# Kernel optimization log

Measured on AMD Instinct MI355X. Metric: run time of the kernel, lower is better.

The kernel has to match this reference:

```python
import jax, jax.numpy as jnp
import numpy as np

B, T, I, H = 64, 188, 512, 1024
R = H  # recurrent_size == hidden_size (required for the cell math to be consistent)


def setup_inputs() -> dict:
    key = jax.random.key(0)
    ks = jax.random.split(key, 6)
    stdv = 1.0 / np.sqrt(H)
    u = lambda k, shape: jax.random.uniform(k, shape, jnp.float32, -stdv, stdv)
    return {
        "x": jax.random.normal(ks[0], (B, T, I), jnp.float32),
        "h0": jnp.zeros((B, R), jnp.float32),
        "c0": jnp.zeros((B, H), jnp.float32),
        "weight_ih": u(ks[1], (4 * H, I)),
        "weight_hh": u(ks[2], (4 * H, R)),
        "weight_rec": u(ks[3], (2 * R, H)),
        "bias": u(ks[4], (4 * H,)),
        "lengths": jax.random.randint(ks[5], (B,), 1, T + 1),
    }


def reference(x, h0, c0, weight_ih, weight_hh, weight_rec, bias, lengths):
    # length_matrix[j][t] == 1 iff t < lengths[j]; state is zeroed where 0
    mask = (jnp.arange(T)[:, None] < lengths[None, :]).astype(x.dtype)[:, :, None]  # [T,B,1]
    # precompute input projections for all timesteps: [T, B, 4H]
    pre_x = jnp.einsum('bti,gi->tbg', x, weight_ih) + bias

    def step(carry, inp):
        h, c = carry
        px, m = inp
        pre = px + h @ weight_hh.T           # [B, 4H]
        pre_c = c @ weight_rec.T             # [B, 2R] (peephole)
        i = jax.nn.sigmoid(pre[:, :H] + pre_c[:, :H])
        f = jax.nn.sigmoid(pre[:, H:2 * H] + pre_c[:, H:2 * H])
        g = jnp.tanh(pre[:, 2 * H:3 * H])
        c_new = f * c + i * g
        o = jax.nn.sigmoid(pre[:, 3 * H:] + c_new)
        h_new = o * jnp.tanh(c_new)
        h_new = h_new * m  # zero finished sequences (index_fill_ with 0)
        c_new = c_new * m
        return (h_new, c_new), (h_new, c_new)

    (_, _), (hs, cs) = jax.lax.scan(step, (h0, c0), (pre_x, mask))
    # stack over time then transpose(0,1) as in torch -> [B, T, H]
    return jnp.swapaxes(hs, 0, 1), jnp.swapaxes(cs, 0, 1)
```

## Files before the change

kernel.cpp:

```cpp
#include <hip/hip_runtime.h>


#define T_N 188

#define WS_PX     0UL
#define WS_XB     98566144UL
#define WS_WIHB   110886912UL
#define WS_WCOMB  115081216UL
#define WS_HST    127664128UL
#define WS_CST    127926272UL
#define WS_FLAGS  128188416UL
#define WS_WRECLO 128192512UL
#define WS_CSTLO  132386816UL

typedef __attribute__((ext_vector_type(8))) short short8;
typedef __attribute__((ext_vector_type(4))) float f4;

__device__ __forceinline__ float b2f(unsigned short u) {
    union { unsigned int i; float f; } v; v.i = ((unsigned int)u) << 16; return v.f;
}
__device__ __forceinline__ unsigned short f2b(float f) {
    unsigned int u = __float_as_uint(f);
    return (unsigned short)((u + 0x7FFFu + ((u >> 16) & 1u)) >> 16);
}
__device__ __forceinline__ float sigf(float x) { return 1.0f / (1.0f + __expf(-x)); }
__device__ __forceinline__ float tanh_(float x) {
    float e = __expf(2.0f * x); return 1.0f - 2.0f / (e + 1.0f);
}
#define MFMA(a, b, c) __builtin_amdgcn_mfma_f32_16x16x32_bf16((a), (b), (c), 0, 0, 0)

#define LD16(dst, addr) \
    asm volatile("global_load_dwordx4 %0, %1, off sc0 sc1" : "=&v"(dst) : "v"(addr))

#define BALLAST(bal)                                                       \
    _Pragma("unroll")                                                      \
    for (int u_ = 0; u_ < 16; ++u_) bal = __builtin_fmaf(bal, 1.0000001f, 1e-7f)

__device__ __forceinline__ f4 px_init(const unsigned short* px, int t, int gate, int jg, int brow) {
    unsigned long long pv =
        *(const unsigned long long*)(px + ((long)(t * 4 + gate) * 1024 + jg) * 64 + brow);
    f4 r;
    r[0] = b2f((unsigned short)pv);
    r[1] = b2f((unsigned short)(pv >> 16));
    r[2] = b2f((unsigned short)(pv >> 32));
    r[3] = b2f((unsigned short)(pv >> 48));
    return r;
}

__global__ void k_prep(const float* __restrict__ x, const float* __restrict__ h0,
                       const float* __restrict__ c0, const float* __restrict__ wih,
                       unsigned short* __restrict__ xb, unsigned short* __restrict__ wihb,
                       unsigned short* __restrict__ hst, unsigned short* __restrict__ cst,
                       unsigned short* __restrict__ cstlo, int* __restrict__ flags) {
    const long NX4 = 1540096, NWIH4 = 524288, NH4 = 16384;
    const long total = NX4 + NWIH4 + NH4 + NH4;
    long gtid = (long)blockIdx.x * blockDim.x + threadIdx.x;
    for (long i = gtid; i < total; i += (long)gridDim.x * blockDim.x) {
        const float* src; unsigned short* dst; unsigned short* lo_dst = nullptr; long off = i;
        if (off < NX4)                  { src = x;   dst = xb; }
        else if ((off -= NX4) < NWIH4)  { src = wih; dst = wihb; }
        else if ((off -= NWIH4) < NH4)  { src = h0;  dst = hst + 65536; }
        else { off -= NH4;                src = c0;  dst = cst + 65536; lo_dst = cstlo + 65536; }
        float4 v = ((const float4*)src)[off];
        unsigned short hx = f2b(v.x), hy = f2b(v.y), hz = f2b(v.z), hw = f2b(v.w);
        unsigned long long o = (unsigned long long)hx
            | ((unsigned long long)hy << 16)
            | ((unsigned long long)hz << 32)
            | ((unsigned long long)hw << 48);
        *(unsigned long long*)(dst + off * 4) = o;
        if (lo_dst) {
            unsigned long long l = (unsigned long long)f2b(v.x - b2f(hx))
                | ((unsigned long long)f2b(v.y - b2f(hy)) << 16)
                | ((unsigned long long)f2b(v.z - b2f(hz)) << 32)
                | ((unsigned long long)f2b(v.w - b2f(hw)) << 48);
            *(unsigned long long*)(lo_dst + off * 4) = l;
        }
    }
    if (gtid < 1024) flags[gtid] = 0;
}

__global__ void __launch_bounds__(256) k_px(const unsigned short* __restrict__ xb,
                                            const unsigned short* __restrict__ wihb,
                                            const float* __restrict__ bias,
                                            unsigned short* __restrict__ px) {
    const int t = blockIdx.y;
    const int wv = threadIdx.x >> 6, lane = threadIdx.x & 63;
    const int col = lane & 15, quad = lane >> 4;
    const int nb = blockIdx.x * 256 + wv * 64;
    f4 acc[4][4];
#pragma unroll
    for (int nt = 0; nt < 4; ++nt) {
        const float bn = bias[nb + nt * 16 + col];
#pragma unroll
        for (int mt = 0; mt < 4; ++mt) {
            acc[mt][nt][0] = bn; acc[mt][nt][1] = bn; acc[mt][nt][2] = bn; acc[mt][nt][3] = bn;
        }
    }
#pragma unroll 4
    for (int kk = 0; kk < 16; ++kk) {
        short8 bf[4], af[4];
#pragma unroll
        for (int nt = 0; nt < 4; ++nt)
            bf[nt] = *(const short8*)(wihb + (nb + nt * 16 + col) * 512 + kk * 32 + quad * 8);
#pragma unroll
        for (int mt = 0; mt < 4; ++mt)
            af[mt] = *(const short8*)(xb + ((mt * 16 + col) * 188 + t) * 512 + kk * 32 + quad * 8);
#pragma unroll
        for (int mt = 0; mt < 4; ++mt)
#pragma unroll
            for (int nt = 0; nt < 4; ++nt)
                acc[mt][nt] = MFMA(af[mt], bf[nt], acc[mt][nt]);
    }
#pragma unroll
    for (int nt = 0; nt < 4; ++nt) {
        const int n = nb + nt * 16 + col;
        const long pb = ((long)(t * 4 + (n >> 10)) * 1024 + (n & 1023)) * 64;
#pragma unroll
        for (int mt = 0; mt < 4; ++mt) {
            unsigned long long o = (unsigned long long)f2b(acc[mt][nt][0])
                | ((unsigned long long)f2b(acc[mt][nt][1]) << 16)
                | ((unsigned long long)f2b(acc[mt][nt][2]) << 32)
                | ((unsigned long long)f2b(acc[mt][nt][3]) << 48);
            *(unsigned long long*)(px + pb + mt * 16 + quad * 4) = o;
        }
    }
}

__global__ void __launch_bounds__(256, 1) k_scan(
    const float* __restrict__ whh, const float* __restrict__ wrec,
    const float* __restrict__ c0, const int* __restrict__ lengths,
    const unsigned short* __restrict__ px, unsigned short* __restrict__ hst,
    unsigned short* __restrict__ cst, unsigned short* __restrict__ cstlo,
    int* __restrict__ flags, float* __restrict__ out) {
    const int cu = blockIdx.x;
    const int g = cu >> 6, cig = cu & 63;
    const int jbase = cig * 16, b0 = g * 16;
    const int tid = threadIdx.x, wv = tid >> 6, lane = tid & 63;
    const int kh = wv >> 1, ts = wv & 1;
    const int kbase = kh * 512;
    const int col = lane & 15, quad = lane >> 4;

    __shared__ float pre[2][2][6][16][16];
    __shared__ float c_loc[16][16];
    __shared__ int go_word;

    short8 wf[4][16];
    if (ts == 0) {
#pragma unroll
        for (int tile = 0; tile < 4; ++tile) {
            const float* src = whh + (long)(tile * 1024 + jbase + col) * 1024 + kbase + quad * 8;
#pragma unroll
            for (int kk = 0; kk < 16; ++kk) {
                float4 a = *(const float4*)(src + kk * 32);
                float4 b = *(const float4*)(src + kk * 32 + 4);
                union { unsigned short u[8]; short8 s; } P;
                P.u[0] = f2b(a.x); P.u[1] = f2b(a.y); P.u[2] = f2b(a.z); P.u[3] = f2b(a.w);
                P.u[4] = f2b(b.x); P.u[5] = f2b(b.y); P.u[6] = f2b(b.z); P.u[7] = f2b(b.w);
                wf[tile][kk] = P.s;
            }
        }
    } else {
#pragma unroll
        for (int tl = 0; tl < 2; ++tl) {
            const float* src = wrec + (long)(tl * 1024 + jbase + col) * 1024 + kbase + quad * 8;
#pragma unroll
            for (int kk = 0; kk < 16; ++kk) {
                float4 a = *(const float4*)(src + kk * 32);
                float4 b = *(const float4*)(src + kk * 32 + 4);
                float w[8] = {a.x, a.y, a.z, a.w, b.x, b.y, b.z, b.w};
                union { unsigned short u[8]; short8 s; } H, L;
#pragma unroll
                for (int e = 0; e < 8; ++e) {
                    unsigned short hi = f2b(w[e]);
                    H.u[e] = hi;
                    L.u[e] = f2b(w[e] - b2f(hi));
                }
                wf[tl][kk] = H.s;
                wf[2 + tl][kk] = L.s;
            }
        }
    }
    {
        int b = tid >> 4, j = tid & 15;
        c_loc[b][j] = c0[(b0 + b) * 1024 + jbase + j];
    }
    if (tid == 0) go_word = 0;
    const int my_len = lengths[b0 + (tid >> 4)];
    float bal = (float)lane + 1.0f;
    __syncthreads();

    float* out_h = out;
    float* out_c = out + 12320768;

    for (int t = 0; t < T_N; ++t) {
        const int sl_r = (t + 1) & 1, sl_w = t & 1, ps = t & 1;

        f4 pxv[4];
        if (ts == 0 && kh == 0) {
#pragma unroll
            for (int tile = 0; tile < 4; ++tile)
                pxv[tile] = px_init(px, t, tile, jbase + col, b0 + quad * 4);
        }

        if (t > 0) {
            if (wv == 0) {
                const int* fp = flags + g * 64 + lane;
                for (;;) {
                    int a = __hip_atomic_load(fp, __ATOMIC_RELAXED, __HIP_MEMORY_SCOPE_AGENT);
                    if (__all(a >= t)) break;
                    BALLAST(bal);
                }
                if (lane == 0)
                    __hip_atomic_store(&go_word, t, __ATOMIC_RELAXED, __HIP_MEMORY_SCOPE_WORKGROUP);
            } else {
                for (;;) {
                    int gw = __hip_atomic_load(&go_word, __ATOMIC_RELAXED, __HIP_MEMORY_SCOPE_WORKGROUP);
                    if (gw >= t) break;
                    BALLAST(bal);
                }
            }
            asm volatile("" ::: "memory");
        }

        const int sbase = sl_r * 65536 + (b0 + col) * 1024 + kbase + quad * 8;

        if (ts == 0) {
            const unsigned short* hp = hst + sbase;
            short8 hbuf[16];
#pragma unroll
            for (int kk = 0; kk < 16; ++kk) LD16(hbuf[kk], hp + kk * 32);
            f4 acc[4];
#pragma unroll
            for (int tile = 0; tile < 4; ++tile) {
                if (kh == 0) acc[tile] = pxv[tile];
                else { acc[tile][0] = 0.f; acc[tile][1] = 0.f; acc[tile][2] = 0.f; acc[tile][3] = 0.f; }
            }
            asm volatile("s_waitcnt vmcnt(0)" ::: "memory");
            __builtin_amdgcn_sched_barrier(0);
#pragma unroll
            for (int kk = 0; kk < 16; ++kk) {
                acc[0] = MFMA(hbuf[kk], wf[0][kk], acc[0]);
                acc[1] = MFMA(hbuf[kk], wf[1][kk], acc[1]);
                acc[2] = MFMA(hbuf[kk], wf[2][kk], acc[2]);
                acc[3] = MFMA(hbuf[kk], wf[3][kk], acc[3]);
            }
#pragma unroll
            for (int tile = 0; tile < 4; ++tile)
#pragma unroll
                for (int r = 0; r < 4; ++r) pre[ps][kh][tile][quad * 4 + r][col] = acc[tile][r];
        } else {
            const unsigned short* cph = cst + sbase;
            const unsigned short* cpl = cstlo + sbase;
            short8 chb[16], clb[16];
#pragma unroll
            for (int kk = 0; kk < 16; ++kk) LD16(chb[kk], cph + kk * 32);
#pragma unroll
            for (int kk = 0; kk < 16; ++kk) LD16(clb[kk], cpl + kk * 32);
            f4 a0 = {0.f, 0.f, 0.f, 0.f}, a1 = a0, a2 = a0, a3 = a0, a4 = a0, a5 = a0;
            asm volatile("s_waitcnt vmcnt(0)" ::: "memory");
            __builtin_amdgcn_sched_barrier(0);
#pragma unroll
            for (int kk = 0; kk < 16; ++kk) {
                a0 = MFMA(chb[kk], wf[0][kk], a0);
                a1 = MFMA(chb[kk], wf[1][kk], a1);
                a2 = MFMA(chb[kk], wf[2][kk], a2);
                a3 = MFMA(chb[kk], wf[3][kk], a3);
                a4 = MFMA(clb[kk], wf[0][kk], a4);
                a5 = MFMA(clb[kk], wf[1][kk], a5);
            }
#pragma unroll
            for (int r = 0; r < 4; ++r) {
                pre[ps][kh][4][quad * 4 + r][col] = a0[r] + a2[r] + a4[r];
                pre[ps][kh][5][quad * 4 + r][col] = a1[r] + a3[r] + a5[r];
            }
        }
        __syncthreads();

        float hn, cn; long ob;
        {
            const int b = tid >> 4, j = tid & 15;
            float pi = pre[ps][0][0][b][j] + pre[ps][1][0][b][j] + pre[ps][0][4][b][j] + pre[ps][1][4][b][j];
            float pf = pre[ps][0][1][b][j] + pre[ps][1][1][b][j] + pre[ps][0][5][b][j] + pre[ps][1][5][b][j];
            float pg = pre[ps][0][2][b][j] + pre[ps][1][2][b][j];
            float po = pre[ps][0][3][b][j] + pre[ps][1][3][b][j];
            const float cprev = c_loc[b][j];
            const float iv = sigf(pi), fv = sigf(pf), gv = tanh_(pg);
            cn = fv * cprev + iv * gv;
            float ov = sigf(po + cn);
            hn = ov * tanh_(cn);
            if (t >= my_len) { hn = 0.f; cn = 0.f; }
            c_loc[b][j] = cn;
            ob = (long)(b0 + b) * 192512 + (long)t * 1024 + jbase + j;
            const int sidx = sl_w * 65536 + (b0 + b) * 1024 + jbase + j;
            unsigned short hb  = f2b(hn);
            unsigned short chb2 = f2b(cn);
            unsigned short clb2 = f2b(cn - b2f(chb2));
            __hip_atomic_store(&hst[sidx],  hb,   __ATOMIC_RELAXED, __HIP_MEMORY_SCOPE_AGENT);
            __hip_atomic_store(&cst[sidx],  chb2, __ATOMIC_RELAXED, __HIP_MEMORY_SCOPE_AGENT);
            __hip_atomic_store(&cstlo[sidx], clb2, __ATOMIC_RELAXED, __HIP_MEMORY_SCOPE_AGENT);
        }
        asm volatile("s_waitcnt vmcnt(0)" ::: "memory");
        __syncthreads();
        if (tid == 0)
            __hip_atomic_store(&flags[cu], t + 1, __ATOMIC_RELAXED, __HIP_MEMORY_SCOPE_AGENT);
        out_h[ob] = hn;
        out_c[ob] = cn;
    }
    asm volatile("" :: "v"(bal));
}

extern "C" void kernel_launch(void* const* d_in, const int* in_sizes, int n_in,
                              void* d_out, int out_size, void* d_ws, size_t ws_size,
                              hipStream_t stream) {
    const float* x    = (const float*)d_in[0];
    const float* h0   = (const float*)d_in[1];
    const float* c0   = (const float*)d_in[2];
    const float* wih  = (const float*)d_in[3];
    const float* whh  = (const float*)d_in[4];
    const float* wrec = (const float*)d_in[5];
    const float* bias = (const float*)d_in[6];
    const int* lengths = (const int*)d_in[7];

    char* ws = (char*)d_ws;
    unsigned short* px     = (unsigned short*)(ws + WS_PX);
    unsigned short* xb     = (unsigned short*)(ws + WS_XB);
    unsigned short* wihb   = (unsigned short*)(ws + WS_WIHB);
    unsigned short* hst    = (unsigned short*)(ws + WS_HST);
    unsigned short* cst    = (unsigned short*)(ws + WS_CST);
    unsigned short* cstlo  = (unsigned short*)(ws + WS_CSTLO);
    int* flags             = (int*)(ws + WS_FLAGS);
    float* out = (float*)d_out;

    hipLaunchKernelGGL(k_prep, dim3(2048), dim3(256), 0, stream,
                       x, h0, c0, wih, xb, wihb, hst, cst, cstlo, flags);
    hipLaunchKernelGGL(k_px, dim3(16, 188), dim3(256), 0, stream, xb, wihb, bias, px);
    hipLaunchKernelGGL(k_scan, dim3(256), dim3(256), 0, stream,
                       whh, wrec, c0, lengths, px, hst, cst, cstlo, flags, out);
}
```

Measured before the change: 1.446 ms.

## Tag state words with generation bits to validate cross-block reads without store fence

Encodes a 2-bit generation tag in the low mantissa bits of every bf16 state word (h hi/lo, c hi/lo). Readers re-load until all tags match the expected generation, so the writer's vmcnt(0) wait before raising the flag can be dropped. It also adds a bf16 low-part split for h, doubling the MFMAs for the recurrent h product to recover the precision lost to the tag bits. The cost is extra loads, extra MFMAs, possible retry spins, and 2 bits less mantissa per half.

```diff
diff --git a/kernel.cpp b/kernel.cpp
--- a/kernel.cpp
+++ b/kernel.cpp
@@ -6,11 +6,10 @@
 #define WS_PX     0UL
 #define WS_XB     98566144UL
 #define WS_WIHB   110886912UL
-#define WS_WCOMB  115081216UL
+#define WS_HSTLO  115081216UL
 #define WS_HST    127664128UL
 #define WS_CST    127926272UL
 #define WS_FLAGS  128188416UL
-#define WS_WRECLO 128192512UL
 #define WS_CSTLO  132386816UL
 
 typedef __attribute__((ext_vector_type(8))) short short8;
@@ -31,6 +30,11 @@
 
 #define LD16(dst, addr) \
     asm volatile("global_load_dwordx4 %0, %1, off sc0 sc1" : "=&v"(dst) : "v"(addr))
+
+__device__ __forceinline__ unsigned int tagxor(short8 v, unsigned int pat) {
+    union { short8 s; unsigned int d[4]; } u; u.s = v;
+    return (u.d[0] ^ pat) | (u.d[1] ^ pat) | (u.d[2] ^ pat) | (u.d[3] ^ pat);
+}
 
 #define BALLAST(bal)                                                       \
     _Pragma("unroll")                                                      \
@@ -50,30 +54,39 @@
 __global__ void k_prep(const float* __restrict__ x, const float* __restrict__ h0,
                        const float* __restrict__ c0, const float* __restrict__ wih,
                        unsigned short* __restrict__ xb, unsigned short* __restrict__ wihb,
-                       unsigned short* __restrict__ hst, unsigned short* __restrict__ cst,
-                       unsigned short* __restrict__ cstlo, int* __restrict__ flags) {
+                       unsigned short* __restrict__ hst, unsigned short* __restrict__ hstlo,
+                       unsigned short* __restrict__ cst, unsigned short* __restrict__ cstlo,
+                       int* __restrict__ flags) {
     const long NX4 = 1540096, NWIH4 = 524288, NH4 = 16384;
     const long total = NX4 + NWIH4 + NH4 + NH4;
     long gtid = (long)blockIdx.x * blockDim.x + threadIdx.x;
     for (long i = gtid; i < total; i += (long)gridDim.x * blockDim.x) {
         const float* src; unsigned short* dst; unsigned short* lo_dst = nullptr; long off = i;
+        bool tag_state = false;
         if (off < NX4)                  { src = x;   dst = xb; }
         else if ((off -= NX4) < NWIH4)  { src = wih; dst = wihb; }
-        else if ((off -= NWIH4) < NH4)  { src = h0;  dst = hst + 65536; }
-        else { off -= NH4;                src = c0;  dst = cst + 65536; lo_dst = cstlo + 65536; }
+        else if ((off -= NWIH4) < NH4)  { src = h0;  dst = hst; lo_dst = hstlo; tag_state = true; }
+        else { off -= NH4;                src = c0;  dst = cst; lo_dst = cstlo; tag_state = true; }
         float4 v = ((const float4*)src)[off];
         unsigned short hx = f2b(v.x), hy = f2b(v.y), hz = f2b(v.z), hw = f2b(v.w);
+        if (tag_state) { hx |= 3u; hy |= 3u; hz |= 3u; hw |= 3u; }
         unsigned long long o = (unsigned long long)hx
             | ((unsigned long long)hy << 16)
             | ((unsigned long long)hz << 32)
             | ((unsigned long long)hw << 48);
         *(unsigned long long*)(dst + off * 4) = o;
+        if (tag_state) *(unsigned long long*)(dst + 65536 + off * 4) = o;
         if (lo_dst) {
-            unsigned long long l = (unsigned long long)f2b(v.x - b2f(hx))
-                | ((unsigned long long)f2b(v.y - b2f(hy)) << 16)
-                | ((unsigned long long)f2b(v.z - b2f(hz)) << 32)
-                | ((unsigned long long)f2b(v.w - b2f(hw)) << 48);
+            unsigned short lx = (unsigned short)(f2b(v.x - b2f(hx)) | 3u);
+            unsigned short ly = (unsigned short)(f2b(v.y - b2f(hy)) | 3u);
+            unsigned short lz = (unsigned short)(f2b(v.z - b2f(hz)) | 3u);
+            unsigned short lw = (unsigned short)(f2b(v.w - b2f(hw)) | 3u);
+            unsigned long long l = (unsigned long long)lx
+                | ((unsigned long long)ly << 16)
+                | ((unsigned long long)lz << 32)
+                | ((unsigned long long)lw << 48);
             *(unsigned long long*)(lo_dst + off * 4) = l;
+            *(unsigned long long*)(lo_dst + 65536 + off * 4) = l;
         }
     }
     if (gtid < 1024) flags[gtid] = 0;
@@ -130,8 +143,9 @@
     const float* __restrict__ whh, const float* __restrict__ wrec,
     const float* __restrict__ c0, const int* __restrict__ lengths,
     const unsigned short* __restrict__ px, unsigned short* __restrict__ hst,
-    unsigned short* __restrict__ cst, unsigned short* __restrict__ cstlo,
-    int* __restrict__ flags, float* __restrict__ out) {
+    unsigned short* __restrict__ hstlo, unsigned short* __restrict__ cst,
+    unsigned short* __restrict__ cstlo, int* __restrict__ flags,
+    float* __restrict__ out) {
     const int cu = blockIdx.x;
     const int g = cu >> 6, cig = cu & 63;
     const int jbase = cig * 16, b0 = g * 16;
@@ -194,6 +208,9 @@
 
     for (int t = 0; t < T_N; ++t) {
         const int sl_r = (t + 1) & 1, sl_w = t & 1, ps = t & 1;
+        const int genr = (t == 0) ? 3 : (((t - 1) >> 1) & 3);
+        const unsigned int pat = (unsigned int)genr * 0x00010001u;
+        const unsigned int gw = (unsigned int)((t >> 1) & 3);
 
         f4 pxv[4];
         if (ts == 0 && kh == 0) {
@@ -214,8 +231,8 @@
                     __hip_atomic_store(&go_word, t, __ATOMIC_RELAXED, __HIP_MEMORY_SCOPE_WORKGROUP);
             } else {
                 for (;;) {
-                    int gw = __hip_atomic_load(&go_word, __ATOMIC_RELAXED, __HIP_MEMORY_SCOPE_WORKGROUP);
-                    if (gw >= t) break;
+                    int gwd = __hip_atomic_load(&go_word, __ATOMIC_RELAXED, __HIP_MEMORY_SCOPE_WORKGROUP);
+                    if (gwd >= t) break;
                     BALLAST(bal);
                 }
             }
@@ -225,18 +242,27 @@
         const int sbase = sl_r * 65536 + (b0 + col) * 1024 + kbase + quad * 8;
 
         if (ts == 0) {
-            const unsigned short* hp = hst + sbase;
-            short8 hbuf[16];
-#pragma unroll
-            for (int kk = 0; kk < 16; ++kk) LD16(hbuf[kk], hp + kk * 32);
+            short8 hbuf[16], hlb[16];
             f4 acc[4];
 #pragma unroll
             for (int tile = 0; tile < 4; ++tile) {
                 if (kh == 0) acc[tile] = pxv[tile];
                 else { acc[tile][0] = 0.f; acc[tile][1] = 0.f; acc[tile][2] = 0.f; acc[tile][3] = 0.f; }
             }
-            asm volatile("s_waitcnt vmcnt(0)" ::: "memory");
-            __builtin_amdgcn_sched_barrier(0);
+            for (;;) {
+#pragma unroll
+                for (int kk = 0; kk < 16; ++kk) LD16(hbuf[kk], hst + sbase + kk * 32);
+#pragma unroll
+                for (int kk = 0; kk < 16; ++kk) LD16(hlb[kk], hstlo + sbase + kk * 32);
+                asm volatile("s_waitcnt vmcnt(0)" ::: "memory");
+                __builtin_amdgcn_sched_barrier(0);
+                unsigned int bad = 0;
+#pragma unroll
+                for (int kk = 0; kk < 16; ++kk)
+                    bad |= tagxor(hbuf[kk], pat) | tagxor(hlb[kk], pat);
+                if (__all((bad & 0x00030003u) == 0u)) break;
+                BALLAST(bal);
+            }
 #pragma unroll
             for (int kk = 0; kk < 16; ++kk) {
                 acc[0] = MFMA(hbuf[kk], wf[0][kk], acc[0]);
@@ -245,20 +271,33 @@
                 acc[3] = MFMA(hbuf[kk], wf[3][kk], acc[3]);
             }
 #pragma unroll
+            for (int kk = 0; kk < 16; ++kk) {
+                acc[0] = MFMA(hlb[kk], wf[0][kk], acc[0]);
+                acc[1] = MFMA(hlb[kk], wf[1][kk], acc[1]);
+                acc[2] = MFMA(hlb[kk], wf[2][kk], acc[2]);
+                acc[3] = MFMA(hlb[kk], wf[3][kk], acc[3]);
+            }
+#pragma unroll
             for (int tile = 0; tile < 4; ++tile)
 #pragma unroll
                 for (int r = 0; r < 4; ++r) pre[ps][kh][tile][quad * 4 + r][col] = acc[tile][r];
         } else {
-            const unsigned short* cph = cst + sbase;
-            const unsigned short* cpl = cstlo + sbase;
             short8 chb[16], clb[16];
-#pragma unroll
-            for (int kk = 0; kk < 16; ++kk) LD16(chb[kk], cph + kk * 32);
-#pragma unroll
-            for (int kk = 0; kk < 16; ++kk) LD16(clb[kk], cpl + kk * 32);
+            for (;;) {
+#pragma unroll
+                for (int kk = 0; kk < 16; ++kk) LD16(chb[kk], cst + sbase + kk * 32);
+#pragma unroll
+                for (int kk = 0; kk < 16; ++kk) LD16(clb[kk], cstlo + sbase + kk * 32);
+                asm volatile("s_waitcnt vmcnt(0)" ::: "memory");
+                __builtin_amdgcn_sched_barrier(0);
+                unsigned int bad = 0;
+#pragma unroll
+                for (int kk = 0; kk < 16; ++kk)
+                    bad |= tagxor(chb[kk], pat) | tagxor(clb[kk], pat);
+                if (__all((bad & 0x00030003u) == 0u)) break;
+                BALLAST(bal);
+            }
             f4 a0 = {0.f, 0.f, 0.f, 0.f}, a1 = a0, a2 = a0, a3 = a0, a4 = a0, a5 = a0;
-            asm volatile("s_waitcnt vmcnt(0)" ::: "memory");
-            __builtin_amdgcn_sched_barrier(0);
 #pragma unroll
             for (int kk = 0; kk < 16; ++kk) {
                 a0 = MFMA(chb[kk], wf[0][kk], a0);
@@ -292,14 +331,15 @@
             c_loc[b][j] = cn;
             ob = (long)(b0 + b) * 192512 + (long)t * 1024 + jbase + j;
             const int sidx = sl_w * 65536 + (b0 + b) * 1024 + jbase + j;
-            unsigned short hb  = f2b(hn);
-            unsigned short chb2 = f2b(cn);
-            unsigned short clb2 = f2b(cn - b2f(chb2));
-            __hip_atomic_store(&hst[sidx],  hb,   __ATOMIC_RELAXED, __HIP_MEMORY_SCOPE_AGENT);
-            __hip_atomic_store(&cst[sidx],  chb2, __ATOMIC_RELAXED, __HIP_MEMORY_SCOPE_AGENT);
-            __hip_atomic_store(&cstlo[sidx], clb2, __ATOMIC_RELAXED, __HIP_MEMORY_SCOPE_AGENT);
-        }
-        asm volatile("s_waitcnt vmcnt(0)" ::: "memory");
+            unsigned short hhw = (unsigned short)((f2b(hn) & 0xFFFCu) | gw);
+            unsigned short hlw = (unsigned short)((f2b(hn - b2f(hhw)) & 0xFFFCu) | gw);
+            unsigned short chw = (unsigned short)((f2b(cn) & 0xFFFCu) | gw);
+            unsigned short clw = (unsigned short)((f2b(cn - b2f(chw)) & 0xFFFCu) | gw);
+            __hip_atomic_store(&hst[sidx],   hhw, __ATOMIC_RELAXED, __HIP_MEMORY_SCOPE_AGENT);
+            __hip_atomic_store(&hstlo[sidx], hlw, __ATOMIC_RELAXED, __HIP_MEMORY_SCOPE_AGENT);
+            __hip_atomic_store(&cst[sidx],   chw, __ATOMIC_RELAXED, __HIP_MEMORY_SCOPE_AGENT);
+            __hip_atomic_store(&cstlo[sidx], clw, __ATOMIC_RELAXED, __HIP_MEMORY_SCOPE_AGENT);
+        }
         __syncthreads();
         if (tid == 0)
             __hip_atomic_store(&flags[cu], t + 1, __ATOMIC_RELAXED, __HIP_MEMORY_SCOPE_AGENT);
@@ -326,14 +366,15 @@
     unsigned short* xb     = (unsigned short*)(ws + WS_XB);
     unsigned short* wihb   = (unsigned short*)(ws + WS_WIHB);
     unsigned short* hst    = (unsigned short*)(ws + WS_HST);
+    unsigned short* hstlo  = (unsigned short*)(ws + WS_HSTLO);
     unsigned short* cst    = (unsigned short*)(ws + WS_CST);
     unsigned short* cstlo  = (unsigned short*)(ws + WS_CSTLO);
     int* flags             = (int*)(ws + WS_FLAGS);
     float* out = (float*)d_out;
 
     hipLaunchKernelGGL(k_prep, dim3(2048), dim3(256), 0, stream,
-                       x, h0, c0, wih, xb, wihb, hst, cst, cstlo, flags);
+                       x, h0, c0, wih, xb, wihb, hst, hstlo, cst, cstlo, flags);
     hipLaunchKernelGGL(k_px, dim3(16, 188), dim3(256), 0, stream, xb, wihb, bias, px);
     hipLaunchKernelGGL(k_scan, dim3(256), dim3(256), 0, stream,
-                       whh, wrec, c0, lengths, px, hst, cst, cstlo, flags, out);
-}
+                       whh, wrec, c0, lengths, px, hst, hstlo, cst, cstlo, flags, out);
+}
```

After: 2.429 ms. +67.9%, slower.
